# Kernel tuning notes

Hardware: AMD Instinct MI355X
Metric: run time of the kernel (lower is better)

## Reference

```python
import jax, jax.numpy as jnp
import numpy as np

HID, FFN, NE, TOPK = 1024, 4096, 8, 2


def setup_inputs() -> dict:
    key = jax.random.key(0)
    ks = jax.random.split(key, 4)
    x = jax.random.normal(ks[0], (2, 2048, HID), dtype=jnp.float32)
    # router: nn.Linear(hidden, num_experts, bias=False), init std=0.02; stored as [H, E]
    Wr = jax.random.normal(ks[1], (HID, NE), dtype=jnp.float32) * 0.02
    # per-expert FFN weights stacked on leading expert axis
    W1 = jax.random.normal(ks[2], (NE, HID, FFN), dtype=jnp.float32) * (1.0 / np.sqrt(HID))
    b1 = jnp.zeros((NE, FFN), dtype=jnp.float32)
    W2 = jax.random.normal(ks[3], (NE, FFN, HID), dtype=jnp.float32) * (1.0 / np.sqrt(FFN))
    b2 = jnp.zeros((NE, HID), dtype=jnp.float32)
    return {"x": x, "Wr": Wr, "W1": W1, "b1": b1, "W2": W2, "b2": b2}


def reference(x, Wr, W1, b1, W2, b2):
    B, S, H = x.shape
    E = Wr.shape[1]
    T = B * S
    xf = x.reshape(T, H)                                  # [T, H]
    logits = xf @ Wr                                      # [T, E]
    probs = jax.nn.softmax(logits, axis=-1)
    topk_p, topk_i = jax.lax.top_k(probs, TOPK)           # [T, K]
    topk_p = topk_p / jnp.sum(topk_p, axis=-1, keepdims=True)
    # dense combine weights: c[t, e] = normalized prob if expert e selected for token t else 0
    c = jnp.zeros((T, E), dtype=xf.dtype).at[jnp.arange(T)[:, None], topk_i].add(topk_p)

    def expert_step(acc, ew):
        w1, bb1, w2, bb2, ce = ew                         # ce: [T]
        h = jax.nn.gelu(xf @ w1 + bb1, approximate=False)  # exact GELU like nn.GELU()
        y = h @ w2 + bb2                                  # [T, H]
        return acc + ce[:, None] * y, None

    out, _ = jax.lax.scan(expert_step, jnp.zeros_like(xf), (W1, b1, W2, b2, c.T))
    return out.reshape(B, S, H)
```

## Files before the change

kernel.cpp:

```cpp
#include <hip/hip_runtime.h>
#include <hip/hip_bf16.h>

#define H 1024
#define F 4096
#define NE 8
#define T 4096

typedef unsigned short u16;
typedef float floatx4 __attribute__((ext_vector_type(4)));
typedef short short8 __attribute__((ext_vector_type(8)));

__device__ __forceinline__ u16 f2bf(float f) {
  union { float f; unsigned int u; } c; c.f = f;
  unsigned int u = c.u;
  return (u16)((u + 0x7fffu + ((u >> 16) & 1u)) >> 16);
}

__device__ __forceinline__ float gelu_f(float x) {
  float x3 = x * x * x;
  float m2y = -1.5957691216f * x - 0.0713548162f * x3;
  float u = __expf(m2y);
  return x * __builtin_amdgcn_rcpf(1.0f + u);
}

__device__ __forceinline__ void load16_lds(const u16* g, u16* l) {
  __builtin_amdgcn_global_load_lds(
      (const __attribute__((address_space(1))) unsigned int*)g,
      (__attribute__((address_space(3))) unsigned int*)l, 16, 0, 0);
}

__global__ __launch_bounds__(256) void router_kernel(
    const float* __restrict__ x, const float* __restrict__ Wr,
    int* __restrict__ cnt, int* __restrict__ tok, float* __restrict__ wgt,
    u16* __restrict__ xb) {
  int t = (blockIdx.x * 256 + threadIdx.x) >> 6;
  int lane = threadIdx.x & 63;
  const float* xr = x + (size_t)t * H;
  double p[NE];
#pragma unroll
  for (int e = 0; e < NE; ++e) p[e] = 0.0;
  for (int k = lane; k < H; k += 64) {
    float xv = xr[k];
    const float4* wr4 = reinterpret_cast<const float4*>(Wr + k * NE);
    float4 a = wr4[0], b = wr4[1];
    p[0] += (double)xv * a.x; p[1] += (double)xv * a.y;
    p[2] += (double)xv * a.z; p[3] += (double)xv * a.w;
    p[4] += (double)xv * b.x; p[5] += (double)xv * b.y;
    p[6] += (double)xv * b.z; p[7] += (double)xv * b.w;
  }
#pragma unroll
  for (int e = 0; e < NE; ++e) {
#pragma unroll
    for (int off = 32; off; off >>= 1) p[e] += __shfl_down(p[e], off, 64);
  }
  if (lane == 0) {
    int i0 = 0;
#pragma unroll
    for (int e = 1; e < NE; ++e) if (p[e] > p[i0]) i0 = e;
    int i1 = (i0 == 0) ? 1 : 0;
#pragma unroll
    for (int e = 0; e < NE; ++e) if (e != i0 && p[e] > p[i1]) i1 = e;
    double d = exp(p[i1] - p[i0]);
    float w0 = (float)(1.0 / (1.0 + d));
    float w1 = (float)(d / (1.0 + d));
    int pos0 = atomicAdd(&cnt[i0], 1);
    tok[i0 * T + pos0] = t; wgt[i0 * T + pos0] = w0;
    int pos1 = atomicAdd(&cnt[i1], 1);
    tok[i1 * T + pos1] = t; wgt[i1 * T + pos1] = w1;
  }
  const float4* xs4 = reinterpret_cast<const float4*>(x + (size_t)blockIdx.x * 4 * H);
  ushort4* xd4 = reinterpret_cast<ushort4*>(xb + (size_t)blockIdx.x * 4 * H);
#pragma unroll
  for (int i = 0; i < 4; ++i) {
    float4 v = xs4[threadIdx.x + i * 256];
    ushort4 o;
    o.x = f2bf(v.x); o.y = f2bf(v.y); o.z = f2bf(v.z); o.w = f2bf(v.w);
    xd4[threadIdx.x + i * 256] = o;
  }
}

__global__ void offsets_kernel(const int* __restrict__ cnt, int* __restrict__ off) {
  if (threadIdx.x == 0) {
    int s = 0;
#pragma unroll
    for (int e = 0; e < NE; ++e) { off[e] = s; s += cnt[e]; }
    off[NE] = s;
  }
}

__global__ __launch_bounds__(256) void transpose_bf16_kernel(
    const float* __restrict__ src, u16* __restrict__ dst, int R, int C) {
  __shared__ u16 tile[64][72];
  int e = blockIdx.z;
  int c0 = blockIdx.x << 6, r0 = blockIdx.y << 6;
  const float* s = src + (size_t)e * R * C;
  u16* d = dst + (size_t)e * R * C;
  int t = threadIdx.x;
  int rl = t >> 4, cl = (t & 15) << 2;
#pragma unroll
  for (int i = 0; i < 4; ++i) {
    float4 v = *reinterpret_cast<const float4*>(&s[(size_t)(r0 + rl + i * 16) * C + c0 + cl]);
    ushort4 o; o.x = f2bf(v.x); o.y = f2bf(v.y); o.z = f2bf(v.z); o.w = f2bf(v.w);
    *reinterpret_cast<ushort4*>(&tile[rl + i * 16][cl]) = o;
  }
  __syncthreads();
  int cl2 = t >> 4, rl2 = (t & 15) << 2;
#pragma unroll
  for (int i = 0; i < 4; ++i) {
    ushort4 o;
    o.x = tile[rl2 + 0][cl2 + i * 16];
    o.y = tile[rl2 + 1][cl2 + i * 16];
    o.z = tile[rl2 + 2][cl2 + i * 16];
    o.w = tile[rl2 + 3][cl2 + i * 16];
    *reinterpret_cast<ushort4*>(&d[(size_t)(c0 + cl2 + i * 16) * R + r0 + rl2]) = o;
  }
}

__global__ __launch_bounds__(256) void gemm1_kernel(
    const u16* __restrict__ Xb, const u16* __restrict__ W1t,
    const float* __restrict__ b1, const int* __restrict__ cnt,
    const int* __restrict__ off, const int* __restrict__ tok,
    u16* __restrict__ Hc) {
  int e = blockIdx.z;
  int n = cnt[e];
  int m0 = blockIdx.y << 7;
  if (m0 >= n) return;
  int n0 = blockIdx.x << 7;
  int rb = off[e];

  __shared__ alignas(16) u16 As[128 * 32];
  __shared__ alignas(16) u16 Bs[128 * 32];
  __shared__ alignas(16) u16 Cs[128][72];
  __shared__ int tokS[128];

  int tid = threadIdx.x;
  if (tid < 128) {
    int s = m0 + tid;
    tokS[tid] = (s < n) ? tok[e * T + s] : 0;
  }
  __syncthreads();

  const u16* W1e = W1t + (size_t)e * F * H;
  const u16* aP0 = Xb + (size_t)tokS[tid >> 2] * H + (tid & 3) * 8;
  const u16* aP1 = Xb + (size_t)tokS[64 + (tid >> 2)] * H + (tid & 3) * 8;
  const u16* bP0 = W1e + (size_t)(n0 + (tid >> 2)) * H + (tid & 3) * 8;
  const u16* bP1 = W1e + (size_t)(n0 + 64 + (tid >> 2)) * H + (tid & 3) * 8;
  u16* aL0 = &As[tid * 8];        u16* aL1 = &As[(tid + 256) * 8];
  u16* bL0 = &Bs[tid * 8];        u16* bL1 = &Bs[(tid + 256) * 8];

  int wv = tid >> 6, lane = tid & 63;
  int wm = wv >> 1, wn = wv & 1;
  int quad = lane >> 4, l16 = lane & 15;

  floatx4 acc[4][4];
#pragma unroll
  for (int mt = 0; mt < 4; ++mt)
#pragma unroll
    for (int nt = 0; nt < 4; ++nt) acc[mt][nt] = floatx4{0.f, 0.f, 0.f, 0.f};

  const u16* aF[4]; const u16* bF[4];
#pragma unroll
  for (int i = 0; i < 4; ++i) {
    aF[i] = &As[(wm * 64 + i * 16 + l16) * 32 + quad * 8];
    bF[i] = &Bs[(wn * 64 + i * 16 + l16) * 32 + quad * 8];
  }

  for (int k0 = 0; k0 < H; k0 += 32) {
    load16_lds(aP0 + k0, aL0);
    load16_lds(aP1 + k0, aL1);
    load16_lds(bP0 + k0, bL0);
    load16_lds(bP1 + k0, bL1);
    __syncthreads();
    short8 av[4], bv[4];
#pragma unroll
    for (int i = 0; i < 4; ++i) {
      av[i] = *reinterpret_cast<const short8*>(aF[i]);
      bv[i] = *reinterpret_cast<const short8*>(bF[i]);
    }
#pragma unroll
    for (int mt = 0; mt < 4; ++mt)
#pragma unroll
      for (int nt = 0; nt < 4; ++nt)
        acc[mt][nt] = __builtin_amdgcn_mfma_f32_16x16x32_bf16(av[mt], bv[nt], acc[mt][nt], 0, 0, 0);
    __syncthreads();
  }

  float b1v[4];
#pragma unroll
  for (int nt = 0; nt < 4; ++nt)
    b1v[nt] = b1[e * F + n0 + wn * 64 + nt * 16 + l16];

#pragma unroll
  for (int p = 0; p < 2; ++p) {
    __syncthreads();
    if (wn == p) {
#pragma unroll
      for (int mt = 0; mt < 4; ++mt)
#pragma unroll
        for (int i = 0; i < 4; ++i) {
          int row = wm * 64 + mt * 16 + quad * 4 + i;
#pragma unroll
          for (int nt = 0; nt < 4; ++nt)
            Cs[row][nt * 16 + l16] = f2bf(gelu_f(acc[mt][nt][i] + b1v[nt]));
        }
    }
    __syncthreads();
    int row = tid >> 1, c0 = (tid & 1) * 32;
    if (m0 + row < n) {
      u16* dst = Hc + (size_t)(rb + m0 + row) * F + n0 + p * 64 + c0;
#pragma unroll
      for (int j = 0; j < 4; ++j)
        *reinterpret_cast<short8*>(dst + j * 8) =
            *reinterpret_cast<const short8*>(&Cs[row][c0 + j * 8]);
    }
  }
}

__global__ __launch_bounds__(256) void gemm2_kernel(
    const u16* __restrict__ Hc, const u16* __restrict__ W2t,
    const float* __restrict__ b2, const int* __restrict__ cnt,
    const int* __restrict__ off, const int* __restrict__ tok,
    const float* __restrict__ wgt, float* __restrict__ out) {
  int e = blockIdx.z >> 1;
  int kh = blockIdx.z & 1;
  int n = cnt[e];
  int m0 = blockIdx.y << 7;
  if (m0 >= n) return;
  int n0 = blockIdx.x << 7;
  int rb = off[e];
  int kbase = kh * (F / 2);

  __shared__ alignas(16) u16 As[128 * 32];
  __shared__ alignas(16) u16 Bs[128 * 32];

  int tid = threadIdx.x;
  const u16* W2e = W2t + (size_t)e * F * H;
  const u16* aP0 = Hc + (size_t)(rb + m0 + (tid >> 2)) * F + kbase + (tid & 3) * 8;
  const u16* aP1 = Hc + (size_t)(rb + m0 + 64 + (tid >> 2)) * F + kbase + (tid & 3) * 8;
  const u16* bP0 = W2e + (size_t)(n0 + (tid >> 2)) * F + kbase + (tid & 3) * 8;
  const u16* bP1 = W2e + (size_t)(n0 + 64 + (tid >> 2)) * F + kbase + (tid & 3) * 8;
  u16* aL0 = &As[tid * 8];        u16* aL1 = &As[(tid + 256) * 8];
  u16* bL0 = &Bs[tid * 8];        u16* bL1 = &Bs[(tid + 256) * 8];

  int wv = tid >> 6, lane = tid & 63;
  int wm = wv >> 1, wn = wv & 1;
  int quad = lane >> 4, l16 = lane & 15;

  floatx4 acc[4][4];
#pragma unroll
  for (int mt = 0; mt < 4; ++mt)
#pragma unroll
    for (int nt = 0; nt < 4; ++nt) acc[mt][nt] = floatx4{0.f, 0.f, 0.f, 0.f};

  const u16* aF[4]; const u16* bF[4];
#pragma unroll
  for (int i = 0; i < 4; ++i) {
    aF[i] = &As[(wm * 64 + i * 16 + l16) * 32 + quad * 8];
    bF[i] = &Bs[(wn * 64 + i * 16 + l16) * 32 + quad * 8];
  }

  for (int k0 = 0; k0 < F / 2; k0 += 32) {
    load16_lds(aP0 + k0, aL0);
    load16_lds(aP1 + k0, aL1);
    load16_lds(bP0 + k0, bL0);
    load16_lds(bP1 + k0, bL1);
    __syncthreads();
    short8 av[4], bv[4];
#pragma unroll
    for (int i = 0; i < 4; ++i) {
      av[i] = *reinterpret_cast<const short8*>(aF[i]);
      bv[i] = *reinterpret_cast<const short8*>(bF[i]);
    }
#pragma unroll
    for (int mt = 0; mt < 4; ++mt)
#pragma unroll
      for (int nt = 0; nt < 4; ++nt)
        acc[mt][nt] = __builtin_amdgcn_mfma_f32_16x16x32_bf16(av[mt], bv[nt], acc[mt][nt], 0, 0, 0);
    __syncthreads();
  }

  float b2v[4];
#pragma unroll
  for (int nt = 0; nt < 4; ++nt)
    b2v[nt] = (kh == 0) ? b2[e * H + n0 + wn * 64 + nt * 16 + l16] : 0.0f;
#pragma unroll
  for (int mt = 0; mt < 4; ++mt) {
#pragma unroll
    for (int i = 0; i < 4; ++i) {
      int row = wm * 64 + mt * 16 + quad * 4 + i;
      int gr = m0 + row;
      if (gr < n) {
        float wv2 = wgt[e * T + gr];
        int tk = tok[e * T + gr];
        float* orow = out + (size_t)tk * H + n0 + wn * 64 + l16;
#pragma unroll
        for (int nt = 0; nt < 4; ++nt)
          atomicAdd(orow + nt * 16, (acc[mt][nt][i] + b2v[nt]) * wv2);
      }
    }
  }
}

extern "C" void kernel_launch(void* const* d_in, const int* in_sizes, int n_in,
                              void* d_out, int out_size, void* d_ws, size_t ws_size,
                              hipStream_t stream) {
  const float* x  = (const float*)d_in[0];
  const float* Wr = (const float*)d_in[1];
  const float* W1 = (const float*)d_in[2];
  const float* b1 = (const float*)d_in[3];
  const float* W2 = (const float*)d_in[4];
  const float* b2 = (const float*)d_in[5];
  float* out = (float*)d_out;

  char* ws = (char*)d_ws;
  int*   cnt = (int*)(ws + 0);
  int*   off = (int*)(ws + 256);
  int*   tok = (int*)(ws + 4096);
  float* wgt = (float*)(ws + 135168);
  u16*   Xb  = (u16*)(ws + 266240);
  u16*   W1t = (u16*)(ws + 8654848);
  u16*   W2t = (u16*)(ws + 75763712);
  u16*   Hc  = (u16*)(ws + 142872576);

  hipMemsetAsync(cnt, 0, 64, stream);
  hipMemsetAsync(out, 0, (size_t)out_size * sizeof(float), stream);

  router_kernel<<<dim3(T / 4), dim3(256), 0, stream>>>(x, Wr, cnt, tok, wgt, Xb);
  offsets_kernel<<<dim3(1), dim3(64), 0, stream>>>(cnt, off);
  transpose_bf16_kernel<<<dim3(F / 64, H / 64, NE), dim3(256), 0, stream>>>(W1, W1t, H, F);
  transpose_bf16_kernel<<<dim3(H / 64, F / 64, NE), dim3(256), 0, stream>>>(W2, W2t, F, H);
  gemm1_kernel<<<dim3(F / 128, 32, NE), dim3(256), 0, stream>>>(Xb, W1t, b1, cnt, off, tok, Hc);
  gemm2_kernel<<<dim3(H / 128, 32, NE * 2), dim3(256), 0, stream>>>(Hc, W2t, b2, cnt, off, tok, wgt, out);
}
```

Baseline: 724.1 us.

## Widen weight transpose tiles, pack bf16 pairs, drop offsets kernel

The fp32-to-bf16 weight transpose now uses 128x128 tiles. Each thread packs two adjacent rows into one 32-bit bf16 pair in LDS, so the transposed output is written with 16-byte stores instead of 8-byte ones. The separate offsets kernel is removed, and each GEMM block computes its expert's row base from the counts. Gemm1's LDS is merged into one shared buffer, and the router's x conversion uses packed bf16 intrinsics. The aim is to cut the bandwidth-bound transpose cost and one kernel launch, at the cost of larger LDS tiles and redundant prefix sums in every block.

New measurement: 719.1 us. No clear change (-0.7%).

```diff
diff --git a/kernel.cpp b/kernel.cpp
--- a/kernel.cpp
+++ b/kernel.cpp
@@ -7,13 +7,19 @@
 #define T 4096
 
 typedef unsigned short u16;
+typedef unsigned int u32;
 typedef float floatx4 __attribute__((ext_vector_type(4)));
 typedef short short8 __attribute__((ext_vector_type(8)));
 
 __device__ __forceinline__ u16 f2bf(float f) {
-  union { float f; unsigned int u; } c; c.f = f;
-  unsigned int u = c.u;
+  union { float f; u32 u; } c; c.f = f;
+  u32 u = c.u;
   return (u16)((u + 0x7fffu + ((u >> 16) & 1u)) >> 16);
+}
+
+__device__ __forceinline__ u32 pkbf(float a, float b) {
+  __hip_bfloat162 h = __float22bfloat162_rn(float2{a, b});
+  u32 r; __builtin_memcpy(&r, &h, 4); return r;
 }
 
 __device__ __forceinline__ float gelu_f(float x) {
@@ -69,69 +75,69 @@
     tok[i1 * T + pos1] = t; wgt[i1 * T + pos1] = w1;
   }
   const float4* xs4 = reinterpret_cast<const float4*>(x + (size_t)blockIdx.x * 4 * H);
-  ushort4* xd4 = reinterpret_cast<ushort4*>(xb + (size_t)blockIdx.x * 4 * H);
+  uint2* xd = reinterpret_cast<uint2*>(xb + (size_t)blockIdx.x * 4 * H);
 #pragma unroll
   for (int i = 0; i < 4; ++i) {
     float4 v = xs4[threadIdx.x + i * 256];
-    ushort4 o;
-    o.x = f2bf(v.x); o.y = f2bf(v.y); o.z = f2bf(v.z); o.w = f2bf(v.w);
-    xd4[threadIdx.x + i * 256] = o;
-  }
-}
-
-__global__ void offsets_kernel(const int* __restrict__ cnt, int* __restrict__ off) {
-  if (threadIdx.x == 0) {
-    int s = 0;
-#pragma unroll
-    for (int e = 0; e < NE; ++e) { off[e] = s; s += cnt[e]; }
-    off[NE] = s;
-  }
-}
-
-__global__ __launch_bounds__(256) void transpose_bf16_kernel(
+    uint2 o; o.x = pkbf(v.x, v.y); o.y = pkbf(v.z, v.w);
+    xd[threadIdx.x + i * 256] = o;
+  }
+}
+
+__global__ __launch_bounds__(256) void transpose_v2_kernel(
     const float* __restrict__ src, u16* __restrict__ dst, int R, int C) {
-  __shared__ u16 tile[64][72];
+  __shared__ u32 tl[64 * 132];
   int e = blockIdx.z;
-  int c0 = blockIdx.x << 6, r0 = blockIdx.y << 6;
+  int r0 = blockIdx.y << 7, c0 = blockIdx.x << 7;
   const float* s = src + (size_t)e * R * C;
   u16* d = dst + (size_t)e * R * C;
-  int t = threadIdx.x;
-  int rl = t >> 4, cl = (t & 15) << 2;
-#pragma unroll
-  for (int i = 0; i < 4; ++i) {
-    float4 v = *reinterpret_cast<const float4*>(&s[(size_t)(r0 + rl + i * 16) * C + c0 + cl]);
-    ushort4 o; o.x = f2bf(v.x); o.y = f2bf(v.y); o.z = f2bf(v.z); o.w = f2bf(v.w);
-    *reinterpret_cast<ushort4*>(&tile[rl + i * 16][cl]) = o;
+  int tid = threadIdx.x;
+  int cq = tid & 31, rp0 = tid >> 5;
+#pragma unroll
+  for (int it = 0; it < 8; ++it) {
+    int rp = rp0 + it * 8;
+    float4 u = *reinterpret_cast<const float4*>(&s[(size_t)(r0 + 2 * rp) * C + c0 + 4 * cq]);
+    float4 v = *reinterpret_cast<const float4*>(&s[(size_t)(r0 + 2 * rp + 1) * C + c0 + 4 * cq]);
+    uint4 q;
+    q.x = pkbf(u.x, v.x); q.y = pkbf(u.y, v.y);
+    q.z = pkbf(u.z, v.z); q.w = pkbf(u.w, v.w);
+    *reinterpret_cast<uint4*>(&tl[rp * 132 + 4 * cq]) = q;
   }
   __syncthreads();
-  int cl2 = t >> 4, rl2 = (t & 15) << 2;
-#pragma unroll
-  for (int i = 0; i < 4; ++i) {
-    ushort4 o;
-    o.x = tile[rl2 + 0][cl2 + i * 16];
-    o.y = tile[rl2 + 1][cl2 + i * 16];
-    o.z = tile[rl2 + 2][cl2 + i * 16];
-    o.w = tile[rl2 + 3][cl2 + i * 16];
-    *reinterpret_cast<ushort4*>(&d[(size_t)(c0 + cl2 + i * 16) * R + r0 + rl2]) = o;
+  int c_l = tid >> 2, rq = tid & 3;
+#pragma unroll
+  for (int pass = 0; pass < 2; ++pass) {
+#pragma unroll
+    for (int it2 = 0; it2 < 4; ++it2) {
+      int c = pass * 64 + c_l;
+      int chunk = rq + 4 * it2;
+      uint4 q;
+      q.x = tl[(4 * chunk + 0) * 132 + c];
+      q.y = tl[(4 * chunk + 1) * 132 + c];
+      q.z = tl[(4 * chunk + 2) * 132 + c];
+      q.w = tl[(4 * chunk + 3) * 132 + c];
+      *reinterpret_cast<uint4*>(&d[(size_t)(c0 + c) * R + r0 + chunk * 8]) = q;
+    }
   }
 }
 
 __global__ __launch_bounds__(256) void gemm1_kernel(
     const u16* __restrict__ Xb, const u16* __restrict__ W1t,
     const float* __restrict__ b1, const int* __restrict__ cnt,
-    const int* __restrict__ off, const int* __restrict__ tok,
-    u16* __restrict__ Hc) {
+    const int* __restrict__ tok, u16* __restrict__ Hc) {
   int e = blockIdx.z;
   int n = cnt[e];
   int m0 = blockIdx.y << 7;
   if (m0 >= n) return;
   int n0 = blockIdx.x << 7;
-  int rb = off[e];
-
-  __shared__ alignas(16) u16 As[128 * 32];
-  __shared__ alignas(16) u16 Bs[128 * 32];
-  __shared__ alignas(16) u16 Cs[128][72];
+  int rb = 0;
+#pragma unroll
+  for (int i = 0; i < NE; ++i) rb += (i < e) ? cnt[i] : 0;
+
+  __shared__ alignas(16) u16 SH[9216];
   __shared__ int tokS[128];
+  u16* As = SH;
+  u16* Bs = SH + 4096;
 
   int tid = threadIdx.x;
   if (tid < 128) {
@@ -201,17 +207,17 @@
           int row = wm * 64 + mt * 16 + quad * 4 + i;
 #pragma unroll
           for (int nt = 0; nt < 4; ++nt)
-            Cs[row][nt * 16 + l16] = f2bf(gelu_f(acc[mt][nt][i] + b1v[nt]));
+            SH[row * 72 + nt * 16 + l16] = f2bf(gelu_f(acc[mt][nt][i] + b1v[nt]));
         }
     }
     __syncthreads();
-    int row = tid >> 1, c0 = (tid & 1) * 32;
+    int row = tid >> 1, cc = (tid & 1) * 32;
     if (m0 + row < n) {
-      u16* dst = Hc + (size_t)(rb + m0 + row) * F + n0 + p * 64 + c0;
+      u16* dst = Hc + (size_t)(rb + m0 + row) * F + n0 + p * 64 + cc;
 #pragma unroll
       for (int j = 0; j < 4; ++j)
         *reinterpret_cast<short8*>(dst + j * 8) =
-            *reinterpret_cast<const short8*>(&Cs[row][c0 + j * 8]);
+            *reinterpret_cast<const short8*>(&SH[row * 72 + cc + j * 8]);
     }
   }
 }
@@ -219,15 +225,17 @@
 __global__ __launch_bounds__(256) void gemm2_kernel(
     const u16* __restrict__ Hc, const u16* __restrict__ W2t,
     const float* __restrict__ b2, const int* __restrict__ cnt,
-    const int* __restrict__ off, const int* __restrict__ tok,
-    const float* __restrict__ wgt, float* __restrict__ out) {
+    const int* __restrict__ tok, const float* __restrict__ wgt,
+    float* __restrict__ out) {
   int e = blockIdx.z >> 1;
   int kh = blockIdx.z & 1;
   int n = cnt[e];
   int m0 = blockIdx.y << 7;
   if (m0 >= n) return;
   int n0 = blockIdx.x << 7;
-  int rb = off[e];
+  int rb = 0;
+#pragma unroll
+  for (int i = 0; i < NE; ++i) rb += (i < e) ? cnt[i] : 0;
   int kbase = kh * (F / 2);
 
   __shared__ alignas(16) u16 As[128 * 32];
@@ -314,7 +322,6 @@
 
   char* ws = (char*)d_ws;
   int*   cnt = (int*)(ws + 0);
-  int*   off = (int*)(ws + 256);
   int*   tok = (int*)(ws + 4096);
   float* wgt = (float*)(ws + 135168);
   u16*   Xb  = (u16*)(ws + 266240);
@@ -326,9 +333,8 @@
   hipMemsetAsync(out, 0, (size_t)out_size * sizeof(float), stream);
 
   router_kernel<<<dim3(T / 4), dim3(256), 0, stream>>>(x, Wr, cnt, tok, wgt, Xb);
-  offsets_kernel<<<dim3(1), dim3(64), 0, stream>>>(cnt, off);
-  transpose_bf16_kernel<<<dim3(F / 64, H / 64, NE), dim3(256), 0, stream>>>(W1, W1t, H, F);
-  transpose_bf16_kernel<<<dim3(H / 64, F / 64, NE), dim3(256), 0, stream>>>(W2, W2t, F, H);
-  gemm1_kernel<<<dim3(F / 128, 32, NE), dim3(256), 0, stream>>>(Xb, W1t, b1, cnt, off, tok, Hc);
-  gemm2_kernel<<<dim3(H / 128, 32, NE * 2), dim3(256), 0, stream>>>(Hc, W2t, b2, cnt, off, tok, wgt, out);
-}
+  transpose_v2_kernel<<<dim3(F / 128, H / 128, NE), dim3(256), 0, stream>>>(W1, W1t, H, F);
+  transpose_v2_kernel<<<dim3(H / 128, F / 128, NE), dim3(256), 0, stream>>>(W2, W2t, F, H);
+  gemm1_kernel<<<dim3(F / 128, 32, NE), dim3(256), 0, stream>>>(Xb, W1t, b1, cnt, tok, Hc);
+  gemm2_kernel<<<dim3(H / 128, 32, NE * 2), dim3(256), 0, stream>>>(Hc, W2t, b2, cnt, tok, wgt, out);
+}
```
